# Kernel tuning notes

Measured on AMD Instinct MI355X. Metric: run time of the kernel, lower is better.

Reference implementation:

```python
import jax, jax.numpy as jnp
import numpy as np

V, E, H, L, B, T = 8192, 64, 256, 2, 4, 512


def setup_inputs() -> dict:
    key = jax.random.key(0)
    ks = jax.random.split(key, 20)
    s = 0.02
    emb = (jax.random.normal(ks[0], (V, E)) * s).at[0].set(0.0)  # padding_idx=0
    x = jax.random.randint(ks[1], (B, T), 0, V)
    return {
        "x": x,
        "emb": emb,
        "W_ih0": jax.random.normal(ks[2], (H, E)) * s,
        "W_hh0": jax.random.normal(ks[3], (H, H)) * s,
        "b_ih0": jnp.zeros((H,), jnp.float32),
        "b_hh0": jnp.zeros((H,), jnp.float32),
        "W_ih1": jax.random.normal(ks[4], (H, H)) * s,
        "W_hh1": jax.random.normal(ks[5], (H, H)) * s,
        "b_ih1": jnp.zeros((H,), jnp.float32),
        "b_hh1": jnp.zeros((H,), jnp.float32),
        "Wq": jax.random.normal(ks[6], (H, H)) * s,
        "Wk": jax.random.normal(ks[7], (H, H)) * s,
        "v": jax.random.normal(ks[8], (H,)) * s,
        "gamma": jnp.ones((2 * H,), jnp.float32),
        "beta": jnp.zeros((2 * H,), jnp.float32),
        "Wfc": jax.random.normal(ks[9], (V, 2 * H)) * s,
        "bfc": jnp.zeros((V,), jnp.float32),
    }


def _rnn_layer(xs, W_ih, W_hh, b_ih, b_hh):
    # xs: (B, T, D) -> ys: (B, T, H), hT: (B, H). Vanilla tanh RNN.
    Bn = xs.shape[0]
    Hn = W_hh.shape[0]
    h0 = jnp.zeros((Bn, Hn), xs.dtype)

    def step(h, xt):
        h_new = jnp.tanh(xt @ W_ih.T + b_ih + h @ W_hh.T + b_hh)
        return h_new, h_new

    hT, ys = jax.lax.scan(step, h0, jnp.swapaxes(xs, 0, 1))
    return jnp.swapaxes(ys, 0, 1), hT


def reference(x, emb, W_ih0, W_hh0, b_ih0, b_hh0, W_ih1, W_hh1, b_ih1, b_hh1,
              Wq, Wk, v, gamma, beta, Wfc, bfc):
    # Dropout layers are identity (eval mode).
    e = emb[x]                                   # (B, T, E)
    y0, h0 = _rnn_layer(e, W_ih0, W_hh0, b_ih0, b_hh0)
    y1, h1 = _rnn_layer(y0, W_ih1, W_hh1, b_ih1, b_hh1)  # (B, T, H)

    # Bahdanau additive attention with causal mask
    q = y1 @ Wq.T                                # (B, T, H)
    k = y1 @ Wk.T                                # (B, T, H)
    # (B, Tq, Tk, H) broadcast add -> tanh -> contract with v
    scores = jnp.einsum('bijh,h->bij', jnp.tanh(q[:, :, None, :] + k[:, None, :, :]), v)
    Tn = scores.shape[1]
    causal = jnp.tril(jnp.ones((Tn, Tn), bool))
    scores = jnp.where(causal[None], scores, jnp.float32(-1e9))
    alpha = jax.nn.softmax(scores, axis=-1)      # (B, Tq, Tk)
    ctx = jnp.einsum('bij,bjh->bih', alpha, y1)  # bmm(alpha, K) with K = rnn_out

    cat = jnp.concatenate([y1, ctx], axis=-1)    # (B, T, 2H)
    mu = cat.mean(-1, keepdims=True)
    var = ((cat - mu) ** 2).mean(-1, keepdims=True)
    normed = (cat - mu) / jnp.sqrt(var + 1e-5) * gamma + beta

    logits = normed @ Wfc.T + bfc                # (B, T, V)
    h = jnp.stack([h0, h1], axis=0)              # (L, B, H)
    return logits, h
```

## Files before the change

### kernel.cpp

```cpp
#include <hip/hip_runtime.h>
#include <hip/hip_bf16.h>

typedef __bf16 bf16x8 __attribute__((ext_vector_type(8)));
typedef float  f32x4  __attribute__((ext_vector_type(4)));
typedef unsigned short u16;

#define T_N 512
#define H_N 256
#define B_N 4
#define V_N 8192
#define E_N 64

__device__ __forceinline__ float tanh_fast(float x) {
    float e = __expf(2.0f * x);
    return 1.0f - __fdividef(2.0f, e + 1.0f);
}

__device__ __forceinline__ float tanh_pade(float x) {
    x = fminf(3.0f, fmaxf(-3.0f, x));
    float x2 = x * x;
    float num = x * (945.0f + x2 * (105.0f + x2));
    float den = 945.0f + x2 * (420.0f + 15.0f * x2);
    return num * __frcp_rn(den);
}

__device__ __forceinline__ u16 f2bf(float f) {
    __hip_bfloat16 h = __float2bfloat16(f);
    return __builtin_bit_cast(u16, h);
}

__device__ __forceinline__ bf16x8 as_bf16x8(uint4 u) {
    return __builtin_bit_cast(bf16x8, u);
}

__device__ __forceinline__ uint4 pack_bf8(f32x4 lo, f32x4 hi) {
    union { u16 s[8]; uint4 u; } r;
    #pragma unroll
    for (int e = 0; e < 4; ++e) { r.s[e] = f2bf(lo[e]); r.s[e+4] = f2bf(hi[e]); }
    return r.u;
}

__device__ __forceinline__ f32x4 mfma16(bf16x8 a, bf16x8 b, f32x4 c) {
    return __builtin_amdgcn_mfma_f32_16x16x32_bf16(a, b, c, 0, 0, 0);
}

__global__ void cvt_bf16_kernel(const float* __restrict__ src, u16* __restrict__ dst, int n4) {
    int i = blockIdx.x * 256 + threadIdx.x;
    if (i < n4) {
        f32x4 v = ((const f32x4*)src)[i];
        union { u16 s[4]; unsigned long long u; } r;
        #pragma unroll
        for (int e = 0; e < 4; ++e) r.s[e] = f2bf(v[e]);
        ((unsigned long long*)dst)[i] = r.u;
    }
}

__global__ __launch_bounds__(256)
void embed_xw0_kernel(const int* __restrict__ x, const float* __restrict__ emb,
                      const float* __restrict__ Wih, const float* __restrict__ bih,
                      const float* __restrict__ bhh, float* __restrict__ xw0) {
    const int t = blockIdx.x, tid = threadIdx.x;
    __shared__ float sE[4][64];
    {
        const int b = tid >> 6, k = tid & 63;
        sE[b][k] = emb[(size_t)x[b * T_N + t] * E_N + k];
    }
    __syncthreads();
    const int j = tid;
    const float* wr = Wih + j * E_N;
    float a0 = 0, a1 = 0, a2 = 0, a3 = 0;
    #pragma unroll 8
    for (int k = 0; k < E_N; ++k) {
        float wv = wr[k];
        a0 += sE[0][k] * wv; a1 += sE[1][k] * wv;
        a2 += sE[2][k] * wv; a3 += sE[3][k] * wv;
    }
    const float bs = bih[j] + bhh[j];
    f32x4 o = { a0 + bs, a1 + bs, a2 + bs, a3 + bs };
    *(f32x4*)(xw0 + ((size_t)t * H_N + j) * 4) = o;
}

__global__ __launch_bounds__(512, 2)
void rnn_fused_kernel(const float* __restrict__ Whh0, const float* __restrict__ Wih1,
                      const float* __restrict__ Whh1, const float* __restrict__ bih1,
                      const float* __restrict__ bhh1, const float* __restrict__ xw0,
                      u16* __restrict__ y1bf, float* __restrict__ y1f,
                      float* __restrict__ hT) {
    __shared__ __align__(16) u16 wih1_lds[128 * 512];
    __shared__ __align__(16) u16 h0buf[2][4][288];
    __shared__ __align__(16) u16 h1buf[2][4][288];

    const int tid = threadIdx.x;
    const int w = tid >> 6, l = tid & 63;
    const int m = l & 15, g = l >> 4, b4 = m & 3;
    const int layer = w >> 2, wl = w & 3;
    const int jmy = (wl << 6) + l;

    for (int idx = tid; idx < 2 * 4 * 288; idx += 512) {
        (&h0buf[0][0][0])[idx] = (u16)0;
        (&h1buf[0][0][0])[idx] = (u16)0;
    }

    for (int f = tid; f < 128 * 64; f += 512) {
        const int grp = f >> 6, lo = f & 63;
        const int jt = grp >> 3, kk = grp & 7;
        const int mo = lo & 15, go = lo >> 4;
        const float* p = Wih1 + (size_t)(jt * 16 + mo) * H_N + (kk << 5) + (go << 3);
        f32x4 lo4 = *(const f32x4*)p;
        f32x4 hi4 = *(const f32x4*)(p + 4);
        *(uint4*)(wih1_lds + (size_t)f * 8) = pack_bf8(lo4, hi4);
    }

    const float* Whh = (layer == 0) ? Whh0 : Whh1;
    bf16x8 wfrag[4][8];
    #pragma unroll
    for (int nt = 0; nt < 4; ++nt) {
        const int j = (wl << 6) + (nt << 4) + m;
        #pragma unroll
        for (int kk = 0; kk < 8; ++kk) {
            const float* p = Whh + (size_t)j * H_N + (kk << 5) + (g << 3);
            f32x4 lo4 = *(const f32x4*)p;
            f32x4 hi4 = *(const f32x4*)(p + 4);
            wfrag[nt][kk] = as_bf16x8(pack_bf8(lo4, hi4));
        }
    }

    const float bias1 = bih1[jmy] + bhh1[jmy];
    const f32x4* xwv = (const f32x4*)xw0;
    f32x4 xw_cur = xwv[jmy];

    __syncthreads();

    for (int it = 0; it < 513; ++it) {
        const int rs = (it & 1) ^ 1;
        if (layer == 0) {
            if (it < 512) {
                const int tn = (it + 1 < 512) ? it + 1 : it;
                f32x4 xw_nxt = xwv[(size_t)tn * H_N + jmy];

                bf16x8 af[8];
                #pragma unroll
                for (int kk = 0; kk < 8; ++kk)
                    af[kk] = as_bf16x8(*(const uint4*)&h0buf[rs][b4][(kk << 5) + (g << 3)]);

                f32x4 ca[4], cb[4];
                #pragma unroll
                for (int nt = 0; nt < 4; ++nt) {
                    ca[nt] = (f32x4){0.f, 0.f, 0.f, 0.f};
                    cb[nt] = (f32x4){0.f, 0.f, 0.f, 0.f};
                }
                #pragma unroll
                for (int kk = 0; kk < 4; ++kk)
                    #pragma unroll
                    for (int nt = 0; nt < 4; ++nt) {
                        ca[nt] = mfma16(af[kk],     wfrag[nt][kk],     ca[nt]);
                        cb[nt] = mfma16(af[kk + 4], wfrag[nt][kk + 4], cb[nt]);
                    }

                f32x4 hv = (g == 0) ? (ca[0] + cb[0])
                         : (g == 1) ? (ca[1] + cb[1])
                         : (g == 2) ? (ca[2] + cb[2])
                         :            (ca[3] + cb[3]);
                hv += xw_cur;

                #pragma unroll
                for (int b = 0; b < 4; ++b) {
                    float hn = tanh_fast(hv[b]);
                    h0buf[it & 1][b][jmy] = f2bf(hn);
                    if (it == T_N - 1) hT[b * H_N + jmy] = hn;
                }
                xw_cur = xw_nxt;
            }
        } else {
            if (it >= 1) {
                const int s = it - 1;
                f32x4 acc[2][4];
                #pragma unroll
                for (int hh = 0; hh < 2; ++hh)
                    #pragma unroll
                    for (int nt = 0; nt < 4; ++nt) acc[hh][nt] = (f32x4){0.f, 0.f, 0.f, 0.f};

                #pragma unroll
                for (int kk = 0; kk < 8; ++kk) {
                    bf16x8 a0 = as_bf16x8(*(const uint4*)&h0buf[rs][b4][(kk << 5) + (g << 3)]);
                    #pragma unroll
                    for (int nt = 0; nt < 4; ++nt) {
                        const int grp = ((wl << 2) + nt) * 8 + kk;
                        bf16x8 bw = as_bf16x8(*(const uint4*)(wih1_lds + ((size_t)grp * 64 + l) * 8));
                        acc[kk >> 2][nt] = mfma16(a0, bw, acc[kk >> 2][nt]);
                    }
                }
                #pragma unroll
                for (int kk = 0; kk < 8; ++kk) {
                    bf16x8 a1 = as_bf16x8(*(const uint4*)&h1buf[rs][b4][(kk << 5) + (g << 3)]);
                    #pragma unroll
                    for (int nt = 0; nt < 4; ++nt)
                        acc[kk >> 2][nt] = mfma16(a1, wfrag[nt][kk], acc[kk >> 2][nt]);
                }

                f32x4 hv = (g == 0) ? (acc[0][0] + acc[1][0])
                         : (g == 1) ? (acc[0][1] + acc[1][1])
                         : (g == 2) ? (acc[0][2] + acc[1][2])
                         :            (acc[0][3] + acc[1][3]);
                hv += (f32x4){bias1, bias1, bias1, bias1};

                #pragma unroll
                for (int b = 0; b < 4; ++b) {
                    float hn = tanh_fast(hv[b]);
                    u16 bits = f2bf(hn);
                    h1buf[it & 1][b][jmy] = bits;
                    y1bf[((size_t)b * T_N + s) * H_N + jmy] = bits;
                    y1f [((size_t)b * T_N + s) * H_N + jmy] = hn;
                    if (s == T_N - 1) hT[1024 + b * H_N + jmy] = hn;
                }
            }
        }
        asm volatile("s_waitcnt lgkmcnt(0)\n\ts_barrier" ::: "memory");
    }
}

template<int MODE>
__global__ __launch_bounds__(256, 2)
void gemm_bf16(const u16* __restrict__ A, const u16* __restrict__ Bw,
               float* __restrict__ out, const float* __restrict__ bias,
               const float* __restrict__ bias2, int M, int N, int K) {
    __shared__ __align__(16) u16 As[64][40];
    __shared__ __align__(16) u16 Bs[64][40];
    const int tid = threadIdx.x;
    const int nb = N >> 6;
    const int bm = blockIdx.x / nb, bn = blockIdx.x % nb;
    const int l = tid & 63, w = tid >> 6;
    const int wm = w & 1, wn = w >> 1;
    const int m = l & 15, g = l >> 4;
    const int srow = tid >> 2, sseg = tid & 3;

    f32x4 c[2][2];
    #pragma unroll
    for (int i = 0; i < 2; ++i)
        #pragma unroll
        for (int j = 0; j < 2; ++j) c[i][j] = (f32x4){0.f, 0.f, 0.f, 0.f};

    const u16* ap = A  + (size_t)(bm * 64 + srow) * K + sseg * 8;
    const u16* bp = Bw + (size_t)(bn * 64 + srow) * K + sseg * 8;

    for (int k0 = 0; k0 < K; k0 += 32) {
        uint4 av = *(const uint4*)(ap + k0);
        uint4 bv = *(const uint4*)(bp + k0);
        __syncthreads();
        *(uint4*)&As[srow][sseg << 3] = av;
        *(uint4*)&Bs[srow][sseg << 3] = bv;
        __syncthreads();
        bf16x8 af[2], bfr[2];
        #pragma unroll
        for (int i = 0; i < 2; ++i) {
            af[i]  = as_bf16x8(*(const uint4*)&As[(wm << 5) + (i << 4) + m][g << 3]);
            bfr[i] = as_bf16x8(*(const uint4*)&Bs[(wn << 5) + (i << 4) + m][g << 3]);
        }
        #pragma unroll
        for (int i = 0; i < 2; ++i)
            #pragma unroll
            for (int j = 0; j < 2; ++j)
                c[i][j] = mfma16(af[i], bfr[j], c[i][j]);
    }

    #pragma unroll
    for (int i = 0; i < 2; ++i)
        #pragma unroll
        for (int j = 0; j < 2; ++j) {
            const int col = (bn << 6) + (wn << 5) + (j << 4) + m;
            float bs = 0.f;
            if (bias)  bs += bias[col];
            if (bias2) bs += bias2[col];
            #pragma unroll
            for (int r = 0; r < 4; ++r) {
                const int row = (bm << 6) + (wm << 5) + (i << 4) + (g << 2) + r;
                const float val = c[i][j][r] + bs;
                if (MODE == 0) {
                    out[(size_t)row * N + col] = val;
                } else {
                    const int b = row >> 9, t = row & 511;
                    out[(size_t)b * N * T_N + (size_t)col * T_N + t] = val;
                }
            }
        }
}

__global__ __launch_bounds__(256, 2)
void gemm_fc(const u16* __restrict__ A, const u16* __restrict__ Bw,
             const float* __restrict__ bias, float* __restrict__ out) {
    __shared__ __align__(16) u16 As[128 * 32];
    __shared__ __align__(16) u16 Bs[128 * 32];
    const int tid = threadIdx.x;
    const int l = tid & 63, w = tid >> 6;
    const int m = l & 15, g = l >> 4;
    const int wm = w >> 1, wn = w & 1;
    const int bm = blockIdx.x >> 6, bn = blockIdx.x & 63;
    constexpr int K = 512;

    f32x4 acc[4][4];
    #pragma unroll
    for (int i = 0; i < 4; ++i)
        #pragma unroll
        for (int j = 0; j < 4; ++j) acc[i][j] = (f32x4){0.f, 0.f, 0.f, 0.f};

    const u16* aBase = A  + (size_t)(bm * 128) * K;
    const u16* bBase = Bw + (size_t)(bn * 128) * K;
    const int row0 = tid >> 2,          seg0 = tid & 3;
    const int row1 = (tid + 256) >> 2,  seg1 = tid & 3;
    const int wseg0 = seg0 ^ ((row0 >> 1) & 3);
    const int wseg1 = seg1 ^ ((row1 >> 1) & 3);

    for (int k0 = 0; k0 < K; k0 += 32) {
        uint4 av0 = *(const uint4*)(aBase + (size_t)row0 * K + k0 + seg0 * 8);
        uint4 av1 = *(const uint4*)(aBase + (size_t)row1 * K + k0 + seg1 * 8);
        uint4 bv0 = *(const uint4*)(bBase + (size_t)row0 * K + k0 + seg0 * 8);
        uint4 bv1 = *(const uint4*)(bBase + (size_t)row1 * K + k0 + seg1 * 8);
        __syncthreads();
        *(uint4*)((char*)As + row0 * 64 + wseg0 * 16) = av0;
        *(uint4*)((char*)As + row1 * 64 + wseg1 * 16) = av1;
        *(uint4*)((char*)Bs + row0 * 64 + wseg0 * 16) = bv0;
        *(uint4*)((char*)Bs + row1 * 64 + wseg1 * 16) = bv1;
        __syncthreads();
        bf16x8 af[4], bfr[4];
        #pragma unroll
        for (int i = 0; i < 4; ++i) {
            const int arow = wm * 64 + i * 16 + m;
            const int aslot = g ^ ((arow >> 1) & 3);
            af[i]  = as_bf16x8(*(const uint4*)((char*)As + arow * 64 + aslot * 16));
            const int brow = wn * 64 + i * 16 + m;
            const int bslot = g ^ ((brow >> 1) & 3);
            bfr[i] = as_bf16x8(*(const uint4*)((char*)Bs + brow * 64 + bslot * 16));
        }
        #pragma unroll
        for (int i = 0; i < 4; ++i)
            #pragma unroll
            for (int j = 0; j < 4; ++j)
                acc[i][j] = mfma16(af[i], bfr[j], acc[i][j]);
    }

    #pragma unroll
    for (int i = 0; i < 4; ++i)
        #pragma unroll
        for (int j = 0; j < 4; ++j) {
            const int col = bn * 128 + wn * 64 + j * 16 + m;
            const float bs = bias[col];
            #pragma unroll
            for (int r = 0; r < 4; ++r) {
                const int row = bm * 128 + wm * 64 + i * 16 + (g << 2) + r;
                out[(size_t)row * V_N + col] = acc[i][j][r] + bs;
            }
        }
}

__global__ __launch_bounds__(256)
void attn_kernel(const float* __restrict__ q, const float* __restrict__ kT,
                 const float* __restrict__ y1f, const float* __restrict__ vvec,
                 float* __restrict__ ctx) {
    const int blk = blockIdx.x;
    const int b = blk >> 9, i = blk & 511;
    const int tid = threadIdx.x;
    __shared__ float sQ[H_N], sV[H_N], sS[T_N];
    __shared__ float red[4];
    sQ[tid] = q[((size_t)b * T_N + i) * H_N + tid];
    sV[tid] = vvec[tid];
    __syncthreads();

    float s0 = -1e30f, s1 = -1e30f;
    if (tid <= i) {
        const float* kp = kT + (size_t)b * H_N * T_N + tid;
        float acc = 0.f;
        for (int h = 0; h < H_N; ++h) acc += sV[h] * tanh_pade(sQ[h] + kp[(size_t)h * T_N]);
        s0 = acc;
    }
    if (tid + 256 <= i) {
        const float* kp = kT + (size_t)b * H_N * T_N + tid + 256;
        float acc = 0.f;
        for (int h = 0; h < H_N; ++h) acc += sV[h] * tanh_pade(sQ[h] + kp[(size_t)h * T_N]);
        s1 = acc;
    }
    float mv = fmaxf(s0, s1);
    #pragma unroll
    for (int o = 32; o; o >>= 1) mv = fmaxf(mv, __shfl_xor(mv, o, 64));
    if ((tid & 63) == 0) red[tid >> 6] = mv;
    __syncthreads();
    mv = fmaxf(fmaxf(red[0], red[1]), fmaxf(red[2], red[3]));
    __syncthreads();
    float e0 = (tid <= i)       ? __expf(s0 - mv) : 0.f;
    float e1 = (tid + 256 <= i) ? __expf(s1 - mv) : 0.f;
    float sm = e0 + e1;
    #pragma unroll
    for (int o = 32; o; o >>= 1) sm += __shfl_xor(sm, o, 64);
    if ((tid & 63) == 0) red[tid >> 6] = sm;
    __syncthreads();
    sm = red[0] + red[1] + red[2] + red[3];
    const float rs = 1.0f / sm;
    sS[tid] = e0 * rs;
    sS[tid + 256] = e1 * rs;
    __syncthreads();
    float acc = 0.f;
    const float* yp = y1f + (size_t)b * T_N * H_N + tid;
    for (int j2 = 0; j2 <= i; ++j2) acc += sS[j2] * yp[(size_t)j2 * H_N];
    ctx[((size_t)b * T_N + i) * H_N + tid] = acc;
}

__global__ __launch_bounds__(256)
void ln_kernel(const float* __restrict__ y1f, const float* __restrict__ ctx,
               const float* __restrict__ gamma, const float* __restrict__ beta,
               u16* __restrict__ outbf) {
    const int row = blockIdx.x, tid = threadIdx.x;
    __shared__ float red[4];
    const float x1 = y1f[(size_t)row * H_N + tid];
    const float x2 = ctx[(size_t)row * H_N + tid];
    float s = x1 + x2;
    #pragma unroll
    for (int o = 32; o; o >>= 1) s += __shfl_xor(s, o, 64);
    if ((tid & 63) == 0) red[tid >> 6] = s;
    __syncthreads();
    const float mu = (red[0] + red[1] + red[2] + red[3]) * (1.f / 512.f);
    __syncthreads();
    const float d1 = x1 - mu, d2 = x2 - mu;
    float qv = d1 * d1 + d2 * d2;
    #pragma unroll
    for (int o = 32; o; o >>= 1) qv += __shfl_xor(qv, o, 64);
    if ((tid & 63) == 0) red[tid >> 6] = qv;
    __syncthreads();
    const float var = (red[0] + red[1] + red[2] + red[3]) * (1.f / 512.f);
    const float inv = rsqrtf(var + 1e-5f);
    outbf[(size_t)row * 512 + tid]       = f2bf(d1 * inv * gamma[tid] + beta[tid]);
    outbf[(size_t)row * 512 + tid + 256] = f2bf(d2 * inv * gamma[tid + 256] + beta[tid + 256]);
}

extern "C" void kernel_launch(void* const* d_in, const int* in_sizes, int n_in,
                              void* d_out, int out_size, void* d_ws, size_t ws_size,
                              hipStream_t stream) {
    const int*   x     = (const int*)  d_in[0];
    const float* emb   = (const float*)d_in[1];
    const float* Wih0  = (const float*)d_in[2];
    const float* Whh0  = (const float*)d_in[3];
    const float* bih0  = (const float*)d_in[4];
    const float* bhh0  = (const float*)d_in[5];
    const float* Wih1  = (const float*)d_in[6];
    const float* Whh1  = (const float*)d_in[7];
    const float* bih1  = (const float*)d_in[8];
    const float* bhh1  = (const float*)d_in[9];
    const float* Wq    = (const float*)d_in[10];
    const float* Wk    = (const float*)d_in[11];
    const float* vvec  = (const float*)d_in[12];
    const float* gamma = (const float*)d_in[13];
    const float* beta  = (const float*)d_in[14];
    const float* Wfc   = (const float*)d_in[15];
    const float* bfc   = (const float*)d_in[16];

    float* outp = (float*)d_out;
    char* ws = (char*)d_ws;
    float* xw0   = (float*)(ws + 0);
    u16*   y1bf  = (u16*)  (ws + 5242880);
    float* y1f   = (float*)(ws + 6291456);
    float* qf    = (float*)(ws + 8388608);
    float* kT    = (float*)(ws + 10485760);
    float* ctx   = (float*)(ws + 12582912);
    u16*   nrm   = (u16*)  (ws + 14680064);
    u16*   Wqb   = (u16*)  (ws + 16908288);
    u16*   Wkb   = (u16*)  (ws + 17039360);
    u16*   Wfcb  = (u16*)  (ws + 17170432);

    float* hout = outp + (size_t)B_N * T_N * V_N;

    cvt_bf16_kernel<<<64,   256, 0, stream>>>(Wq,  Wqb,  65536 / 4);
    cvt_bf16_kernel<<<64,   256, 0, stream>>>(Wk,  Wkb,  65536 / 4);
    cvt_bf16_kernel<<<4096, 256, 0, stream>>>(Wfc, Wfcb, 4194304 / 4);

    embed_xw0_kernel<<<512, 256, 0, stream>>>(x, emb, Wih0, bih0, bhh0, xw0);
    rnn_fused_kernel<<<1, 512, 0, stream>>>(Whh0, Wih1, Whh1, bih1, bhh1,
                                            xw0, y1bf, y1f, hout);
    gemm_bf16<0><<<32 * 4, 256, 0, stream>>>(y1bf, Wqb, qf, nullptr, nullptr, 2048, 256, 256);
    gemm_bf16<2><<<32 * 4, 256, 0, stream>>>(y1bf, Wkb, kT, nullptr, nullptr, 2048, 256, 256);
    attn_kernel<<<2048, 256, 0, stream>>>(qf, kT, y1f, vvec, ctx);
    ln_kernel<<<2048, 256, 0, stream>>>(y1f, ctx, gamma, beta, nrm);
    gemm_fc<<<16 * 64, 256, 0, stream>>>(nrm, Wfcb, bfc, outp);
}
```

Measured before the change: 915.3 us.

## Batch layer-1 input projection over 4 timesteps off the recurrence critical path

The layer-1 W_ih1·h0 product is removed from the per-step critical path. Every 4 steps, all 8 waves cooperatively compute it for 4 timesteps at once (M=16 rows = 4 steps × 4 batch) using a ring buffer of layer-0 outputs and pre-packed bf16 weights streamed from global memory. Layer 1 now lags 5 steps and its per-step work becomes an 8-deep MFMA chain like layer 0. This trades the 64 KB LDS weight copy and extra serial MFMAs for a periodic burst step with global loads, which adds latency on those iterations.

```diff
diff --git a/kernel.cpp b/kernel.cpp
--- a/kernel.cpp
+++ b/kernel.cpp
@@ -53,6 +53,17 @@
         for (int e = 0; e < 4; ++e) r.s[e] = f2bf(v[e]);
         ((unsigned long long*)dst)[i] = r.u;
     }
+}
+
+__global__ __launch_bounds__(256)
+void prep_wih1_kernel(const float* __restrict__ Wih1, uint4* __restrict__ out) {
+    const int f = blockIdx.x * 256 + threadIdx.x;
+    const int jt = f >> 9, kk = (f >> 6) & 7, lo = f & 63;
+    const int mo = lo & 15, go = lo >> 4;
+    const float* p = Wih1 + (size_t)(jt * 16 + mo) * H_N + (kk << 5) + (go << 3);
+    f32x4 a = *(const f32x4*)p;
+    f32x4 b = *(const f32x4*)(p + 4);
+    out[f] = pack_bf8(a, b);
 }
 
 __global__ __launch_bounds__(256)
@@ -81,14 +92,14 @@
 }
 
 __global__ __launch_bounds__(512, 2)
-void rnn_fused_kernel(const float* __restrict__ Whh0, const float* __restrict__ Wih1,
-                      const float* __restrict__ Whh1, const float* __restrict__ bih1,
+void rnn_fused_kernel(const float* __restrict__ Whh0, const float* __restrict__ Whh1,
+                      const uint4* __restrict__ xfg, const float* __restrict__ bih1,
                       const float* __restrict__ bhh1, const float* __restrict__ xw0,
                       u16* __restrict__ y1bf, float* __restrict__ y1f,
                       float* __restrict__ hT) {
-    __shared__ __align__(16) u16 wih1_lds[128 * 512];
-    __shared__ __align__(16) u16 h0buf[2][4][288];
-    __shared__ __align__(16) u16 h1buf[2][4][288];
+    __shared__ __align__(16) u16   ring[8][4][264];
+    __shared__ __align__(16) u16   h1b[2][4][264];
+    __shared__ __align__(16) float xwb[2][4][256][4];
 
     const int tid = threadIdx.x;
     const int w = tid >> 6, l = tid & 63;
@@ -96,20 +107,8 @@
     const int layer = w >> 2, wl = w & 3;
     const int jmy = (wl << 6) + l;
 
-    for (int idx = tid; idx < 2 * 4 * 288; idx += 512) {
-        (&h0buf[0][0][0])[idx] = (u16)0;
-        (&h1buf[0][0][0])[idx] = (u16)0;
-    }
-
-    for (int f = tid; f < 128 * 64; f += 512) {
-        const int grp = f >> 6, lo = f & 63;
-        const int jt = grp >> 3, kk = grp & 7;
-        const int mo = lo & 15, go = lo >> 4;
-        const float* p = Wih1 + (size_t)(jt * 16 + mo) * H_N + (kk << 5) + (go << 3);
-        f32x4 lo4 = *(const f32x4*)p;
-        f32x4 hi4 = *(const f32x4*)(p + 4);
-        *(uint4*)(wih1_lds + (size_t)f * 8) = pack_bf8(lo4, hi4);
-    }
+    for (int i = tid; i < 8 * 4 * 264; i += 512) (&ring[0][0][0])[i] = (u16)0;
+    for (int i = tid; i < 2 * 4 * 264; i += 512) (&h1b[0][0][0])[i] = (u16)0;
 
     const float* Whh = (layer == 0) ? Whh0 : Whh1;
     bf16x8 wfrag[4][8];
@@ -128,20 +127,29 @@
     const float bias1 = bih1[jmy] + bhh1[jmy];
     const f32x4* xwv = (const f32x4*)xw0;
     f32x4 xw_cur = xwv[jmy];
-
-    __syncthreads();
-
-    for (int it = 0; it < 513; ++it) {
-        const int rs = (it & 1) ^ 1;
+    const uint4* xgw = xfg + ((size_t)w << 10);
+
+    __syncthreads();
+
+    for (int it = 0; it < 517; ++it) {
+        const bool burst = ((it & 3) == 0) && (it >= 4) && (it <= 512);
+
+        uint4 xf0[8];
+        if (burst) {
+            #pragma unroll
+            for (int kk = 0; kk < 8; ++kk) xf0[kk] = xgw[(kk << 6) + l];
+        }
+
         if (layer == 0) {
             if (it < 512) {
                 const int tn = (it + 1 < 512) ? it + 1 : it;
                 f32x4 xw_nxt = xwv[(size_t)tn * H_N + jmy];
+                const int rs = (it - 1) & 7;
 
                 bf16x8 af[8];
                 #pragma unroll
                 for (int kk = 0; kk < 8; ++kk)
-                    af[kk] = as_bf16x8(*(const uint4*)&h0buf[rs][b4][(kk << 5) + (g << 3)]);
+                    af[kk] = as_bf16x8(*(const uint4*)&ring[rs][b4][(kk << 5) + (g << 3)]);
 
                 f32x4 ca[4], cb[4];
                 #pragma unroll
@@ -166,55 +174,82 @@
                 #pragma unroll
                 for (int b = 0; b < 4; ++b) {
                     float hn = tanh_fast(hv[b]);
-                    h0buf[it & 1][b][jmy] = f2bf(hn);
+                    ring[it & 7][b][jmy] = f2bf(hn);
                     if (it == T_N - 1) hT[b * H_N + jmy] = hn;
                 }
                 xw_cur = xw_nxt;
             }
         } else {
-            if (it >= 1) {
-                const int s = it - 1;
-                f32x4 acc[2][4];
-                #pragma unroll
-                for (int hh = 0; hh < 2; ++hh)
-                    #pragma unroll
-                    for (int nt = 0; nt < 4; ++nt) acc[hh][nt] = (f32x4){0.f, 0.f, 0.f, 0.f};
-
-                #pragma unroll
-                for (int kk = 0; kk < 8; ++kk) {
-                    bf16x8 a0 = as_bf16x8(*(const uint4*)&h0buf[rs][b4][(kk << 5) + (g << 3)]);
+            if (it >= 5) {
+                const int s = it - 5;
+                f32x4 xws = *(const f32x4*)&xwb[(s >> 2) & 1][s & 3][jmy][0];
+                const int rs = (s - 1) & 1;
+
+                bf16x8 af[8];
+                #pragma unroll
+                for (int kk = 0; kk < 8; ++kk)
+                    af[kk] = as_bf16x8(*(const uint4*)&h1b[rs][b4][(kk << 5) + (g << 3)]);
+
+                f32x4 ca[4], cb[4];
+                #pragma unroll
+                for (int nt = 0; nt < 4; ++nt) {
+                    ca[nt] = (f32x4){0.f, 0.f, 0.f, 0.f};
+                    cb[nt] = (f32x4){0.f, 0.f, 0.f, 0.f};
+                }
+                #pragma unroll
+                for (int kk = 0; kk < 4; ++kk)
                     #pragma unroll
                     for (int nt = 0; nt < 4; ++nt) {
-                        const int grp = ((wl << 2) + nt) * 8 + kk;
-                        bf16x8 bw = as_bf16x8(*(const uint4*)(wih1_lds + ((size_t)grp * 64 + l) * 8));
-                        acc[kk >> 2][nt] = mfma16(a0, bw, acc[kk >> 2][nt]);
+                        ca[nt] = mfma16(af[kk],     wfrag[nt][kk],     ca[nt]);
+                        cb[nt] = mfma16(af[kk + 4], wfrag[nt][kk + 4], cb[nt]);
                     }
-                }
-                #pragma unroll
-                for (int kk = 0; kk < 8; ++kk) {
-                    bf16x8 a1 = as_bf16x8(*(const uint4*)&h1buf[rs][b4][(kk << 5) + (g << 3)]);
-                    #pragma unroll
-                    for (int nt = 0; nt < 4; ++nt)
-                        acc[kk >> 2][nt] = mfma16(a1, wfrag[nt][kk], acc[kk >> 2][nt]);
-                }
-
-                f32x4 hv = (g == 0) ? (acc[0][0] + acc[1][0])
-                         : (g == 1) ? (acc[0][1] + acc[1][1])
-                         : (g == 2) ? (acc[0][2] + acc[1][2])
-                         :            (acc[0][3] + acc[1][3]);
+
+                f32x4 hv = (g == 0) ? (ca[0] + cb[0])
+                         : (g == 1) ? (ca[1] + cb[1])
+                         : (g == 2) ? (ca[2] + cb[2])
+                         :            (ca[3] + cb[3]);
+                hv += xws;
                 hv += (f32x4){bias1, bias1, bias1, bias1};
 
                 #pragma unroll
                 for (int b = 0; b < 4; ++b) {
                     float hn = tanh_fast(hv[b]);
                     u16 bits = f2bf(hn);
-                    h1buf[it & 1][b][jmy] = bits;
+                    h1b[s & 1][b][jmy] = bits;
                     y1bf[((size_t)b * T_N + s) * H_N + jmy] = bits;
                     y1f [((size_t)b * T_N + s) * H_N + jmy] = hn;
                     if (s == T_N - 1) hT[1024 + b * H_N + jmy] = hn;
                 }
             }
         }
+
+        if (burst) {
+            const int t0 = it - 4;
+            const int par = ((it - 4) >> 2) & 1;
+            const int slotm = (t0 + (m >> 2)) & 7;
+            bf16x8 ax[8];
+            #pragma unroll
+            for (int kk = 0; kk < 8; ++kk)
+                ax[kk] = as_bf16x8(*(const uint4*)&ring[slotm][b4][(kk << 5) + (g << 3)]);
+
+            f32x4 xa0 = {0.f, 0.f, 0.f, 0.f};
+            #pragma unroll
+            for (int kk = 0; kk < 8; ++kk)
+                xa0 = mfma16(ax[kk], as_bf16x8(xf0[kk]), xa0);
+
+            uint4 xf1[8];
+            #pragma unroll
+            for (int kk = 0; kk < 8; ++kk) xf1[kk] = xgw[512 + (kk << 6) + l];
+
+            f32x4 xa1 = {0.f, 0.f, 0.f, 0.f};
+            #pragma unroll
+            for (int kk = 0; kk < 8; ++kk)
+                xa1 = mfma16(ax[kk], as_bf16x8(xf1[kk]), xa1);
+
+            *(f32x4*)&xwb[par][g][(w << 5) + m][0]      = xa0;
+            *(f32x4*)&xwb[par][g][(w << 5) + 16 + m][0] = xa1;
+        }
+
         asm volatile("s_waitcnt lgkmcnt(0)\n\ts_barrier" ::: "memory");
     }
 }
@@ -454,6 +489,7 @@
     float* outp = (float*)d_out;
     char* ws = (char*)d_ws;
     float* xw0   = (float*)(ws + 0);
+    uint4* xfg   = (uint4*)(ws + 2097152);
     u16*   y1bf  = (u16*)  (ws + 5242880);
     float* y1f   = (float*)(ws + 6291456);
     float* qf    = (float*)(ws + 8388608);
@@ -469,9 +505,10 @@
     cvt_bf16_kernel<<<64,   256, 0, stream>>>(Wq,  Wqb,  65536 / 4);
     cvt_bf16_kernel<<<64,   256, 0, stream>>>(Wk,  Wkb,  65536 / 4);
     cvt_bf16_kernel<<<4096, 256, 0, stream>>>(Wfc, Wfcb, 4194304 / 4);
+    prep_wih1_kernel<<<32, 256, 0, stream>>>(Wih1, xfg);
 
     embed_xw0_kernel<<<512, 256, 0, stream>>>(x, emb, Wih0, bih0, bhh0, xw0);
-    rnn_fused_kernel<<<1, 512, 0, stream>>>(Whh0, Wih1, Whh1, bih1, bhh1,
+    rnn_fused_kernel<<<1, 512, 0, stream>>>(Whh0, Whh1, xfg, bih1, bhh1,
                                             xw0, y1bf, y1f, hout);
     gemm_bf16<0><<<32 * 4, 256, 0, stream>>>(y1bf, Wqb, qf, nullptr, nullptr, 2048, 256, 256);
     gemm_bf16<2><<<32 * 4, 256, 0, stream>>>(y1bf, Wkb, kT, nullptr, nullptr, 2048, 256, 256);
```

Measured after the change: 876.5 us. 4.2% less time.
